# Optimization experiments

Measured on AMD Instinct MI355X. Metric: run time of the kernel, lower is better.

The kernel has to match this reference:

```python
import jax, jax.numpy as jnp
import numpy as np

B, C, L = 4, 192, 4096
DIV = 3
CO = C // DIV  # 64


def setup_inputs() -> dict:
    key = jax.random.key(0)
    ks = jax.random.split(key, 6)
    # kaiming-normal-ish init for 1x1 conv weights, stored as (out, in) matrices
    std = float(np.sqrt(2.0 / C))
    return {
        "x": jax.random.normal(ks[0], (B, C, L, 1), dtype=jnp.float32),
        "Wq": jax.random.normal(ks[1], (CO, C), dtype=jnp.float32) * std,
        "Wk": jax.random.normal(ks[2], (CO, C), dtype=jnp.float32) * std,
        "Wv": jax.random.normal(ks[3], (CO, C), dtype=jnp.float32) * std,
        "Wv1": jax.random.normal(ks[4], (CO, C), dtype=jnp.float32) * std,
        "gamma": jnp.zeros((1,), dtype=jnp.float32) + 0.5,  # nonzero so attn path is exercised
    }


def reference(x, Wq, Wk, Wv, Wv1, gamma):
    b, c, l, _ = x.shape
    xf = x.reshape(b, c, l)                      # (B, C, L)
    f = jnp.einsum("oc,bcl->bol", Wq, xf)        # (B, CO, L)
    g = jnp.einsum("oc,bcl->bol", Wk, xf)
    h = jnp.einsum("oc,bcl->bol", Wv, xf)
    v1 = jnp.einsum("oc,bcl->bol", Wv1, xf)
    # scores[b, l, m] = sum_o f[b,o,l] * g[b,o,m]; softmax over dim=1 (l axis)
    scores = jnp.einsum("bol,bom->blm", f, g)    # (B, L, L)
    beta = jax.nn.softmax(scores, axis=1)
    o = gamma * jnp.einsum("bol,blm->bom", h, beta) + v1  # (B, CO, L)
    return o.reshape(b, c // 3, l, 1)
```

## Files before the change

### kernel.cpp

```cpp
#include <hip/hip_runtime.h>
#include <math.h>

#define B_ 4
#define C_ 192
#define L_ 4096
#define CO_ 64
#define LOG2E 1.44269504088896340736f

using half8 = __attribute__((ext_vector_type(8))) _Float16;
using half4v = __attribute__((ext_vector_type(4))) _Float16;
using half2v = __attribute__((ext_vector_type(2))) _Float16;
using f32x16 = __attribute__((ext_vector_type(16))) float;

#if __has_builtin(__builtin_amdgcn_exp2f)
#define EXP2(x) __builtin_amdgcn_exp2f(x)
#else
#define EXP2(x) exp2f(x)
#endif

__device__ inline half2v pkrtz(float a, float b) {
  return __builtin_bit_cast(half2v, __builtin_amdgcn_cvt_pkrtz(a, b));
}

union U32H2 { int i; half2v h; };
__device__ inline half2v shfl32(half2v v) {
  U32H2 u; u.h = v;
  u.i = __shfl_xor(u.i, 32, 64);
  return u.h;
}


__global__ void wcvt_kernel(const float* __restrict__ Wq,
                            const float* __restrict__ Wk,
                            const float* __restrict__ Wv,
                            const float* __restrict__ Wv1,
                            _Float16* __restrict__ Wf) {
  const float* src = (blockIdx.y == 0) ? Wq
                     : (blockIdx.y == 1) ? Wk
                     : (blockIdx.y == 2) ? Wv : Wv1;
  const float s = (blockIdx.y == 0) ? LOG2E : 1.0f;
  const int idx = (blockIdx.x * 256 + threadIdx.x) * 4;
  if (idx < CO_ * C_) {
    const float4 v = *(const float4*)(src + idx);
    half4v h;
    h[0] = (_Float16)(v.x * s); h[1] = (_Float16)(v.y * s);
    h[2] = (_Float16)(v.z * s); h[3] = (_Float16)(v.w * s);
    *(half4v*)(Wf + (size_t)blockIdx.y * CO_ * C_ + idx) = h;
  }
}

__global__ __launch_bounds__(256) void proj_mfma(
    const float* __restrict__ x, const _Float16* __restrict__ Wf,
    _Float16* __restrict__ fB, _Float16* __restrict__ gB,
    _Float16* __restrict__ hB, float* __restrict__ v1N) {
  __shared__ __align__(16) float xs[C_ * 32];
  const int b = blockIdx.y, l0 = blockIdx.x * 32;
  const int t = threadIdx.x;
  const int lane = t & 63, w = t >> 6;
  const int m = lane & 31, hi = lane >> 5;

  {
    const float* xb = x + (size_t)b * C_ * L_ + l0;
    const int c0 = w * 48;
#pragma unroll
    for (int i = 0; i < 6; ++i) {
      const int cc = c0 + i * 8;
      const float* gp = xb + (size_t)(cc + (lane >> 3)) * L_ + (lane & 7) * 4;
      __builtin_amdgcn_global_load_lds(
          (const __attribute__((address_space(1))) void*)gp,
          (__attribute__((address_space(3))) void*)&xs[cc * 32], 16, 0, 0);
    }
  }
  __syncthreads();

  const _Float16* Wp = Wf + (size_t)w * CO_ * C_;
  if (w < 2) {
    f32x16 acc0 = {}, acc1 = {};
#pragma unroll
    for (int ks = 0; ks < 12; ++ks) {
      const float* xr = &xs[(ks * 16 + hi * 8) * 32 + m];
      half8 aF;
#pragma unroll
      for (int e = 0; e < 8; e += 2) {
        const half2v hp = pkrtz(xr[e * 32], xr[(e + 1) * 32]);
        aF[e] = hp[0]; aF[e + 1] = hp[1];
      }
      const half8 b0 = *(const half8*)(Wp + (size_t)m * C_ + ks * 16 + hi * 8);
      const half8 b1 =
          *(const half8*)(Wp + (size_t)(32 + m) * C_ + ks * 16 + hi * 8);
      acc0 = __builtin_amdgcn_mfma_f32_32x32x16_f16(aF, b0, acc0, 0, 0, 0);
      acc1 = __builtin_amdgcn_mfma_f32_32x32x16_f16(aF, b1, acc1, 0, 0, 0);
    }
    _Float16* dst = (w == 0) ? fB : gB;
#pragma unroll
    for (int r = 0; r < 16; ++r) {
      const int lrow = 4 * hi + 8 * (r >> 2) + (r & 3);
      _Float16* row = dst + ((size_t)b * L_ + l0 + lrow) * CO_;
      row[m] = (_Float16)acc0[r];
      row[32 + m] = (_Float16)acc1[r];
    }
  } else {
    const int lg = l0 + m;
    for (int oh = 0; oh < 2; ++oh) {
      const _Float16* wr = Wp + (size_t)(32 * oh + m) * C_ + hi * 8;
      f32x16 acc = {};
#pragma unroll
      for (int ks = 0; ks < 12; ++ks) {
        const float* xr = &xs[(16 * ks + 8 * hi) * 32 + m];
        half8 bF;
#pragma unroll
        for (int e = 0; e < 8; e += 2) {
          const half2v hp = pkrtz(xr[e * 32], xr[(e + 1) * 32]);
          bF[e] = hp[0]; bF[e + 1] = hp[1];
        }
        const half8 aF = *(const half8*)(wr + ks * 16);
        acc = __builtin_amdgcn_mfma_f32_32x32x16_f16(aF, bF, acc, 0, 0, 0);
      }
      if (w == 2) {
#pragma unroll
        for (int r = 0; r < 16; ++r) {
          const int o = 32 * oh + 4 * hi + 8 * (r >> 2) + (r & 3);
          hB[((size_t)b * CO_ + o) * L_ + lg] = (_Float16)acc[r];
        }
      } else {
#pragma unroll
        for (int r = 0; r < 16; ++r) {
          const int o = 32 * oh + 4 * hi + 8 * (r >> 2) + (r & 3);
          v1N[((size_t)b * CO_ + o) * L_ + lg] = acc[r];
        }
      }
    }
  }
}

__device__ __forceinline__ void softmax_o(const f32x16& S, float& mx, float& Z,
                                          f32x16& oa, f32x16& ob,
                                          const half8* hc, bool h1) {
  float tmax = S[0];
#pragma unroll
  for (int r = 1; r < 16; ++r) tmax = fmaxf(tmax, S[r]);
  tmax = fmaxf(tmax, __shfl_xor(tmax, 32, 64));
  if (__any(tmax > mx)) {
    const float mnew = fmaxf(mx, tmax);
    const float corr = EXP2(mx - mnew);
    mx = mnew;
    Z *= corr;
#pragma unroll
    for (int r = 0; r < 16; ++r) { oa[r] *= corr; ob[r] *= corr; }
  }
  half2v q[8];
  float zl = 0.f;
#pragma unroll
  for (int j = 0; j < 8; ++j) {
    const float p0 = EXP2(S[2 * j] - mx);
    const float p1 = EXP2(S[2 * j + 1] - mx);
    zl += p0 + p1;
    q[j] = pkrtz(p0, p1);
  }
  Z += zl;
  half2v sq[8];
#pragma unroll
  for (int j = 0; j < 8; ++j) sq[j] = shfl32(q[j]);
  const half2v c0 = h1 ? sq[2] : q[0];
  const half2v c1 = h1 ? sq[3] : q[1];
  const half2v c2 = h1 ? q[2] : sq[0];
  const half2v c3 = h1 ? q[3] : sq[1];
  const half2v c4 = h1 ? sq[6] : q[4];
  const half2v c5 = h1 ? sq[7] : q[5];
  const half2v c6 = h1 ? q[6] : sq[4];
  const half2v c7 = h1 ? q[7] : sq[5];
  half8 bP0, bP1;
  bP0[0] = c0[0]; bP0[1] = c0[1]; bP0[2] = c1[0]; bP0[3] = c1[1];
  bP0[4] = c2[0]; bP0[5] = c2[1]; bP0[6] = c3[0]; bP0[7] = c3[1];
  bP1[0] = c4[0]; bP1[1] = c4[1]; bP1[2] = c5[0]; bP1[3] = c5[1];
  bP1[4] = c6[0]; bP1[5] = c6[1]; bP1[6] = c7[0]; bP1[7] = c7[1];
  oa = __builtin_amdgcn_mfma_f32_32x32x16_f16(hc[0], bP0, oa, 0, 0, 0);
  oa = __builtin_amdgcn_mfma_f32_32x32x16_f16(hc[1], bP1, oa, 0, 0, 0);
  ob = __builtin_amdgcn_mfma_f32_32x32x16_f16(hc[2], bP0, ob, 0, 0, 0);
  ob = __builtin_amdgcn_mfma_f32_32x32x16_f16(hc[3], bP1, ob, 0, 0, 0);
}

__global__ __launch_bounds__(512, 2) void attn_mfma(
    const _Float16* __restrict__ fB, const _Float16* __restrict__ gB,
    const _Float16* __restrict__ hB, const float* __restrict__ v1N,
    const float* __restrict__ gamma_p, float* __restrict__ out) {
  __shared__ float obuf4[4][CO_][65];
  __shared__ float redM[8][64];
  __shared__ float redZ[8][64];

  const int id = blockIdx.x;
  const int b = (id >> 1) & 3;
  const int mt = ((id & 1) << 5) | (id >> 3);
  const int m0 = mt * 64;
  const int t = threadIdx.x;
  const int lane = t & 63, s = t >> 6;
  const int m = lane & 31, hi = lane >> 5;
  const bool h1 = (hi != 0);

  const _Float16* fBase = fB + (size_t)b * L_ * CO_;
  const _Float16* hBase = hB + (size_t)b * CO_ * L_;

  const _Float16* g0 = gB + ((size_t)b * L_ + m0 + m) * CO_ + hi * 8;
  const _Float16* g1 = g0 + (size_t)32 * CO_;
  half8 gf0[4], gf1[4];
#pragma unroll
  for (int ks = 0; ks < 4; ++ks) {
    gf0[ks] = *(const half8*)(g0 + ks * 16);
    gf1[ks] = *(const half8*)(g1 + ks * 16);
  }

  f32x16 o0 = {}, o1 = {}, o2 = {}, o3 = {};
  float mx0 = -1e30f, Z0 = 0.f, mx1 = -1e30f, Z1 = 0.f;

  const int lbase = s * 512;
  half8 fc[2][4], hc[2][4];
  {
    const _Float16* fr = fBase + (size_t)(lbase + m) * CO_ + hi * 8;
#pragma unroll
    for (int ks = 0; ks < 4; ++ks) fc[0][ks] = *(const half8*)(fr + ks * 16);
    const _Float16* hr = hBase + (size_t)m * L_ + lbase + hi * 8;
    const _Float16* hr2 = hr + (size_t)32 * L_;
    hc[0][0] = *(const half8*)(hr);
    hc[0][1] = *(const half8*)(hr + 16);
    hc[0][2] = *(const half8*)(hr2);
    hc[0][3] = *(const half8*)(hr2 + 16);
  }

#pragma unroll 2
  for (int stp = 0; stp < 16; ++stp) {
    const int cur = stp & 1, nxt = cur ^ 1;
    const int lb = lbase + stp * 32;
    {
      const int ln = lb + 32;
      const _Float16* fr = fBase + (size_t)(ln + m) * CO_ + hi * 8;
#pragma unroll
      for (int ks = 0; ks < 4; ++ks) fc[nxt][ks] = *(const half8*)(fr + ks * 16);
      const _Float16* hr = hBase + (size_t)m * L_ + ln + hi * 8;
      const _Float16* hr2 = hr + (size_t)32 * L_;
      hc[nxt][0] = *(const half8*)(hr);
      hc[nxt][1] = *(const half8*)(hr + 16);
      hc[nxt][2] = *(const half8*)(hr2);
      hc[nxt][3] = *(const half8*)(hr2 + 16);
    }
    f32x16 S0 = {}, S1 = {};
#pragma unroll
    for (int ks = 0; ks < 4; ++ks) {
      S0 = __builtin_amdgcn_mfma_f32_32x32x16_f16(fc[cur][ks], gf0[ks], S0, 0, 0, 0);
      S1 = __builtin_amdgcn_mfma_f32_32x32x16_f16(fc[cur][ks], gf1[ks], S1, 0, 0, 0);
    }
    softmax_o(S0, mx0, Z0, o0, o1, hc[cur], h1);
    softmax_o(S1, mx1, Z1, o2, o3, hc[cur], h1);
  }

  Z0 += __shfl_xor(Z0, 32, 64);
  Z1 += __shfl_xor(Z1, 32, 64);
  if (hi == 0) {
    redM[s][m] = mx0; redM[s][m + 32] = mx1;
    redZ[s][m] = Z0;  redZ[s][m + 32] = Z1;
  }
  __syncthreads();
  float M0 = redM[0][m], M1 = redM[0][m + 32];
#pragma unroll
  for (int i = 1; i < 8; ++i) {
    M0 = fmaxf(M0, redM[i][m]);
    M1 = fmaxf(M1, redM[i][m + 32]);
  }
  const float sc0 = EXP2(mx0 - M0);
  const float sc1 = EXP2(mx1 - M1);
  if (s < 4) {
#pragma unroll
    for (int r = 0; r < 16; ++r) {
      const int o = 4 * hi + 8 * (r >> 2) + (r & 3);
      obuf4[s][o][m] = sc0 * o0[r];
      obuf4[s][o + 32][m] = sc0 * o1[r];
      obuf4[s][o][m + 32] = sc1 * o2[r];
      obuf4[s][o + 32][m + 32] = sc1 * o3[r];
    }
  }
  __syncthreads();
  if (s >= 4) {
#pragma unroll
    for (int r = 0; r < 16; ++r) {
      const int o = 4 * hi + 8 * (r >> 2) + (r & 3);
      obuf4[s - 4][o][m] += sc0 * o0[r];
      obuf4[s - 4][o + 32][m] += sc0 * o1[r];
      obuf4[s - 4][o][m + 32] += sc1 * o2[r];
      obuf4[s - 4][o + 32][m + 32] += sc1 * o3[r];
    }
  }
  __syncthreads();

  const float gam = gamma_p[0];
  const int me = t & 63;
  const int og = t >> 6;
  float M = redM[0][me];
#pragma unroll
  for (int i = 1; i < 8; ++i) M = fmaxf(M, redM[i][me]);
  float Zt = 0.f;
#pragma unroll
  for (int i = 0; i < 8; ++i) Zt += EXP2(redM[i][me] - M) * redZ[i][me];
  const float inv = 1.0f / Zt;
#pragma unroll
  for (int i = 0; i < 8; ++i) {
    const int o = og * 8 + i;
    const float val = obuf4[0][o][me] + obuf4[1][o][me] +
                      obuf4[2][o][me] + obuf4[3][o][me];
    const size_t g = ((size_t)b * CO_ + o) * L_ + m0 + me;
    out[g] = gam * val * inv + v1N[g];
  }
}

extern "C" void kernel_launch(void* const* d_in, const int* in_sizes, int n_in,
                              void* d_out, int out_size, void* d_ws,
                              size_t ws_size, hipStream_t stream) {
  const float* x = (const float*)d_in[0];
  const float* Wq = (const float*)d_in[1];
  const float* Wk = (const float*)d_in[2];
  const float* Wv = (const float*)d_in[3];
  const float* Wv1 = (const float*)d_in[4];
  const float* gamma = (const float*)d_in[5];
  float* out = (float*)d_out;

  _Float16* Wf = (_Float16*)d_ws;
  _Float16* fB = Wf + (size_t)4 * CO_ * C_;
  _Float16* gB = fB + (size_t)B_ * L_ * CO_;
  _Float16* hB = gB + (size_t)B_ * L_ * CO_;
  float* v1N = (float*)(hB + (size_t)B_ * L_ * CO_);

  wcvt_kernel<<<dim3(12, 4), 256, 0, stream>>>(Wq, Wk, Wv, Wv1, Wf);
  proj_mfma<<<dim3(L_ / 32, B_), 256, 0, stream>>>(x, Wf, fB, gB, hB, v1N);
  attn_mfma<<<256, 512, 0, stream>>>(fB, gB, hB, v1N, gamma, out);
}
```

Before: 118.7 us.

## Pre-pack f, h and weights into MFMA fragment layout; stage P through LDS

Weights are converted into a lane-major MFMA fragment layout so each lane loads a contiguous half8. The projection kernel also writes f and h in that tile-packed layout through LDS staging, so the attention kernel can read them with fully coalesced per-lane loads. In the attention loop, the cross-half shuffle and select shuffle that built the P operand is replaced by writing P to a per-wave LDS scratch and reading it back as B-operand fragments. This trades VALU shuffle work for LDS traffic and adds extra LDS in both kernels, which may affect occupancy.

```diff
diff --git a/kernel.cpp b/kernel.cpp
--- a/kernel.cpp
+++ b/kernel.cpp
@@ -22,39 +22,41 @@
   return __builtin_bit_cast(half2v, __builtin_amdgcn_cvt_pkrtz(a, b));
 }
 
-union U32H2 { int i; half2v h; };
-__device__ inline half2v shfl32(half2v v) {
-  U32H2 u; u.h = v;
-  u.i = __shfl_xor(u.i, 32, 64);
-  return u.h;
-}
-
-
-__global__ void wcvt_kernel(const float* __restrict__ Wq,
-                            const float* __restrict__ Wk,
-                            const float* __restrict__ Wv,
-                            const float* __restrict__ Wv1,
-                            _Float16* __restrict__ Wf) {
-  const float* src = (blockIdx.y == 0) ? Wq
-                     : (blockIdx.y == 1) ? Wk
-                     : (blockIdx.y == 2) ? Wv : Wv1;
-  const float s = (blockIdx.y == 0) ? LOG2E : 1.0f;
-  const int idx = (blockIdx.x * 256 + threadIdx.x) * 4;
-  if (idx < CO_ * C_) {
-    const float4 v = *(const float4*)(src + idx);
-    half4v h;
-    h[0] = (_Float16)(v.x * s); h[1] = (_Float16)(v.y * s);
-    h[2] = (_Float16)(v.z * s); h[3] = (_Float16)(v.w * s);
-    *(half4v*)(Wf + (size_t)blockIdx.y * CO_ * C_ + idx) = h;
-  }
+
+__global__ __launch_bounds__(256) void wpack_kernel(
+    const float* __restrict__ Wq, const float* __restrict__ Wk,
+    const float* __restrict__ Wv, const float* __restrict__ Wv1,
+    _Float16* __restrict__ Wpack) {
+  const int tid = blockIdx.x * 256 + threadIdx.x;
+  const int w = tid / 1536;
+  const int rem = tid % 1536;
+  const int og = rem / 768;
+  const int ks = (rem % 768) / 64;
+  const int lane = rem % 64;
+  const float* src = (w == 0) ? Wq : (w == 1) ? Wk : (w == 2) ? Wv : Wv1;
+  const float s = (w == 0) ? LOG2E : 1.0f;
+  const int row = og * 32 + (lane & 31);
+  const int col = ks * 16 + (lane >> 5) * 8;
+  const float* p = src + row * C_ + col;
+  const float4 a = *(const float4*)(p);
+  const float4 c = *(const float4*)(p + 4);
+  half8 o;
+  half2v t;
+  t = pkrtz(a.x * s, a.y * s); o[0] = t[0]; o[1] = t[1];
+  t = pkrtz(a.z * s, a.w * s); o[2] = t[0]; o[3] = t[1];
+  t = pkrtz(c.x * s, c.y * s); o[4] = t[0]; o[5] = t[1];
+  t = pkrtz(c.z * s, c.w * s); o[6] = t[0]; o[7] = t[1];
+  *(half8*)(Wpack + (size_t)tid * 8) = o;
 }
 
 __global__ __launch_bounds__(256) void proj_mfma(
-    const float* __restrict__ x, const _Float16* __restrict__ Wf,
-    _Float16* __restrict__ fB, _Float16* __restrict__ gB,
-    _Float16* __restrict__ hB, float* __restrict__ v1N) {
+    const float* __restrict__ x, const _Float16* __restrict__ Wpack,
+    _Float16* __restrict__ fPack, _Float16* __restrict__ gB,
+    _Float16* __restrict__ hPack, float* __restrict__ v1N) {
   __shared__ __align__(16) float xs[C_ * 32];
-  const int b = blockIdx.y, l0 = blockIdx.x * 32;
+  __shared__ __align__(16) _Float16 fl[32 * 72];
+  __shared__ __align__(16) _Float16 hl[64 * 40];
+  const int b = blockIdx.y, T = blockIdx.x, l0 = T * 32;
   const int t = threadIdx.x;
   const int lane = t & 63, w = t >> 6;
   const int m = lane & 31, hi = lane >> 5;
@@ -73,7 +75,14 @@
   }
   __syncthreads();
 
-  const _Float16* Wp = Wf + (size_t)w * CO_ * C_;
+  const _Float16* Wp = Wpack + (size_t)w * 1536 * 8;
+  half8 wf[2][12];
+#pragma unroll
+  for (int og = 0; og < 2; ++og)
+#pragma unroll
+    for (int ks = 0; ks < 12; ++ks)
+      wf[og][ks] = *(const half8*)(Wp + ((size_t)(og * 12 + ks) * 64 + lane) * 8);
+
   if (w < 2) {
     f32x16 acc0 = {}, acc1 = {};
 #pragma unroll
@@ -85,24 +94,35 @@
         const half2v hp = pkrtz(xr[e * 32], xr[(e + 1) * 32]);
         aF[e] = hp[0]; aF[e + 1] = hp[1];
       }
-      const half8 b0 = *(const half8*)(Wp + (size_t)m * C_ + ks * 16 + hi * 8);
-      const half8 b1 =
-          *(const half8*)(Wp + (size_t)(32 + m) * C_ + ks * 16 + hi * 8);
-      acc0 = __builtin_amdgcn_mfma_f32_32x32x16_f16(aF, b0, acc0, 0, 0, 0);
-      acc1 = __builtin_amdgcn_mfma_f32_32x32x16_f16(aF, b1, acc1, 0, 0, 0);
-    }
-    _Float16* dst = (w == 0) ? fB : gB;
-#pragma unroll
-    for (int r = 0; r < 16; ++r) {
-      const int lrow = 4 * hi + 8 * (r >> 2) + (r & 3);
-      _Float16* row = dst + ((size_t)b * L_ + l0 + lrow) * CO_;
-      row[m] = (_Float16)acc0[r];
-      row[32 + m] = (_Float16)acc1[r];
+      acc0 = __builtin_amdgcn_mfma_f32_32x32x16_f16(aF, wf[0][ks], acc0, 0, 0, 0);
+      acc1 = __builtin_amdgcn_mfma_f32_32x32x16_f16(aF, wf[1][ks], acc1, 0, 0, 0);
+    }
+    if (w == 0) {
+#pragma unroll
+      for (int r = 0; r < 16; ++r) {
+        const int l = 4 * hi + 8 * (r >> 2) + (r & 3);
+        fl[l * 72 + m] = (_Float16)acc0[r];
+        fl[l * 72 + 32 + m] = (_Float16)acc1[r];
+      }
+      _Float16* dst = fPack + (size_t)b * L_ * CO_ + (size_t)T * 4 * 64 * 8;
+#pragma unroll
+      for (int ks = 0; ks < 4; ++ks) {
+        const half8 v = *(const half8*)&fl[(lane & 31) * 72 + ks * 16 + (lane >> 5) * 8];
+        *(half8*)(dst + ((size_t)ks * 64 + lane) * 8) = v;
+      }
+    } else {
+      _Float16* dst = gB;
+#pragma unroll
+      for (int r = 0; r < 16; ++r) {
+        const int lrow = 4 * hi + 8 * (r >> 2) + (r & 3);
+        _Float16* row = dst + ((size_t)b * L_ + l0 + lrow) * CO_;
+        row[m] = (_Float16)acc0[r];
+        row[32 + m] = (_Float16)acc1[r];
+      }
     }
   } else {
     const int lg = l0 + m;
     for (int oh = 0; oh < 2; ++oh) {
-      const _Float16* wr = Wp + (size_t)(32 * oh + m) * C_ + hi * 8;
       f32x16 acc = {};
 #pragma unroll
       for (int ks = 0; ks < 12; ++ks) {
@@ -113,14 +133,13 @@
           const half2v hp = pkrtz(xr[e * 32], xr[(e + 1) * 32]);
           bF[e] = hp[0]; bF[e + 1] = hp[1];
         }
-        const half8 aF = *(const half8*)(wr + ks * 16);
-        acc = __builtin_amdgcn_mfma_f32_32x32x16_f16(aF, bF, acc, 0, 0, 0);
+        acc = __builtin_amdgcn_mfma_f32_32x32x16_f16(wf[oh][ks], bF, acc, 0, 0, 0);
       }
       if (w == 2) {
 #pragma unroll
         for (int r = 0; r < 16; ++r) {
           const int o = 32 * oh + 4 * hi + 8 * (r >> 2) + (r & 3);
-          hB[((size_t)b * CO_ + o) * L_ + lg] = (_Float16)acc[r];
+          hl[o * 40 + m] = (_Float16)acc[r];
         }
       } else {
 #pragma unroll
@@ -130,12 +149,23 @@
         }
       }
     }
+    if (w == 2) {
+      _Float16* dst = hPack + (size_t)b * L_ * CO_ + (size_t)T * 4 * 64 * 8;
+#pragma unroll
+      for (int j = 0; j < 4; ++j) {
+        const int oh2 = j >> 1, ks2 = j & 1;
+        const half8 v = *(const half8*)&hl[(32 * oh2 + (lane & 31)) * 40 +
+                                           ks2 * 16 + (lane >> 5) * 8];
+        *(half8*)(dst + ((size_t)j * 64 + lane) * 8) = v;
+      }
+    }
   }
 }
 
 __device__ __forceinline__ void softmax_o(const f32x16& S, float& mx, float& Z,
                                           f32x16& oa, f32x16& ob,
-                                          const half8* hc, bool h1) {
+                                          const half8* hc, _Float16* Pw,
+                                          int m, int hi) {
   float tmax = S[0];
 #pragma unroll
   for (int r = 1; r < 16; ++r) tmax = fmaxf(tmax, S[r]);
@@ -148,32 +178,22 @@
 #pragma unroll
     for (int r = 0; r < 16; ++r) { oa[r] *= corr; ob[r] *= corr; }
   }
-  half2v q[8];
   float zl = 0.f;
 #pragma unroll
-  for (int j = 0; j < 8; ++j) {
-    const float p0 = EXP2(S[2 * j] - mx);
-    const float p1 = EXP2(S[2 * j + 1] - mx);
-    zl += p0 + p1;
-    q[j] = pkrtz(p0, p1);
+  for (int u = 0; u < 4; ++u) {
+    const float p0 = EXP2(S[4 * u + 0] - mx);
+    const float p1 = EXP2(S[4 * u + 1] - mx);
+    const float p2 = EXP2(S[4 * u + 2] - mx);
+    const float p3 = EXP2(S[4 * u + 3] - mx);
+    zl += (p0 + p1) + (p2 + p3);
+    const half2v lo = pkrtz(p0, p1);
+    const half2v hi2 = pkrtz(p2, p3);
+    half4v w4; w4[0] = lo[0]; w4[1] = lo[1]; w4[2] = hi2[0]; w4[3] = hi2[1];
+    *(half4v*)(Pw + m * 40 + 4 * hi + 8 * u) = w4;
   }
   Z += zl;
-  half2v sq[8];
-#pragma unroll
-  for (int j = 0; j < 8; ++j) sq[j] = shfl32(q[j]);
-  const half2v c0 = h1 ? sq[2] : q[0];
-  const half2v c1 = h1 ? sq[3] : q[1];
-  const half2v c2 = h1 ? q[2] : sq[0];
-  const half2v c3 = h1 ? q[3] : sq[1];
-  const half2v c4 = h1 ? sq[6] : q[4];
-  const half2v c5 = h1 ? sq[7] : q[5];
-  const half2v c6 = h1 ? q[6] : sq[4];
-  const half2v c7 = h1 ? q[7] : sq[5];
-  half8 bP0, bP1;
-  bP0[0] = c0[0]; bP0[1] = c0[1]; bP0[2] = c1[0]; bP0[3] = c1[1];
-  bP0[4] = c2[0]; bP0[5] = c2[1]; bP0[6] = c3[0]; bP0[7] = c3[1];
-  bP1[0] = c4[0]; bP1[1] = c4[1]; bP1[2] = c5[0]; bP1[3] = c5[1];
-  bP1[4] = c6[0]; bP1[5] = c6[1]; bP1[6] = c7[0]; bP1[7] = c7[1];
+  const half8 bP0 = *(const half8*)(Pw + m * 40 + 8 * hi);
+  const half8 bP1 = *(const half8*)(Pw + m * 40 + 16 + 8 * hi);
   oa = __builtin_amdgcn_mfma_f32_32x32x16_f16(hc[0], bP0, oa, 0, 0, 0);
   oa = __builtin_amdgcn_mfma_f32_32x32x16_f16(hc[1], bP1, oa, 0, 0, 0);
   ob = __builtin_amdgcn_mfma_f32_32x32x16_f16(hc[2], bP0, ob, 0, 0, 0);
@@ -181,9 +201,10 @@
 }
 
 __global__ __launch_bounds__(512, 2) void attn_mfma(
-    const _Float16* __restrict__ fB, const _Float16* __restrict__ gB,
-    const _Float16* __restrict__ hB, const float* __restrict__ v1N,
+    const _Float16* __restrict__ fPack, const _Float16* __restrict__ gB,
+    const _Float16* __restrict__ hPack, const float* __restrict__ v1N,
     const float* __restrict__ gamma_p, float* __restrict__ out) {
+  __shared__ __align__(16) _Float16 Pl[8][32 * 40];
   __shared__ float obuf4[4][CO_][65];
   __shared__ float redM[8][64];
   __shared__ float redZ[8][64];
@@ -195,10 +216,10 @@
   const int t = threadIdx.x;
   const int lane = t & 63, s = t >> 6;
   const int m = lane & 31, hi = lane >> 5;
-  const bool h1 = (hi != 0);
-
-  const _Float16* fBase = fB + (size_t)b * L_ * CO_;
-  const _Float16* hBase = hB + (size_t)b * CO_ * L_;
+
+  const _Float16* fT = fPack + (size_t)b * L_ * CO_;
+  const _Float16* hT = hPack + (size_t)b * L_ * CO_;
+  _Float16* Pw = &Pl[s][0];
 
   const _Float16* g0 = gB + ((size_t)b * L_ + m0 + m) * CO_ + hi * 8;
   const _Float16* g1 = g0 + (size_t)32 * CO_;
@@ -212,35 +233,30 @@
   f32x16 o0 = {}, o1 = {}, o2 = {}, o3 = {};
   float mx0 = -1e30f, Z0 = 0.f, mx1 = -1e30f, Z1 = 0.f;
 
-  const int lbase = s * 512;
+  const int T0 = s * 16;
   half8 fc[2][4], hc[2][4];
   {
-    const _Float16* fr = fBase + (size_t)(lbase + m) * CO_ + hi * 8;
-#pragma unroll
-    for (int ks = 0; ks < 4; ++ks) fc[0][ks] = *(const half8*)(fr + ks * 16);
-    const _Float16* hr = hBase + (size_t)m * L_ + lbase + hi * 8;
-    const _Float16* hr2 = hr + (size_t)32 * L_;
-    hc[0][0] = *(const half8*)(hr);
-    hc[0][1] = *(const half8*)(hr + 16);
-    hc[0][2] = *(const half8*)(hr2);
-    hc[0][3] = *(const half8*)(hr2 + 16);
+    const _Float16* fp = fT + ((size_t)T0 * 4 * 64 + lane) * 8;
+    const _Float16* hp = hT + ((size_t)T0 * 4 * 64 + lane) * 8;
+#pragma unroll
+    for (int ks = 0; ks < 4; ++ks) {
+      fc[0][ks] = *(const half8*)(fp + (size_t)ks * 64 * 8);
+      hc[0][ks] = *(const half8*)(hp + (size_t)ks * 64 * 8);
+    }
   }
 
 #pragma unroll 2
   for (int stp = 0; stp < 16; ++stp) {
     const int cur = stp & 1, nxt = cur ^ 1;
-    const int lb = lbase + stp * 32;
     {
-      const int ln = lb + 32;
-      const _Float16* fr = fBase + (size_t)(ln + m) * CO_ + hi * 8;
-#pragma unroll
-      for (int ks = 0; ks < 4; ++ks) fc[nxt][ks] = *(const half8*)(fr + ks * 16);
-      const _Float16* hr = hBase + (size_t)m * L_ + ln + hi * 8;
-      const _Float16* hr2 = hr + (size_t)32 * L_;
-      hc[nxt][0] = *(const half8*)(hr);
-      hc[nxt][1] = *(const half8*)(hr + 16);
-      hc[nxt][2] = *(const half8*)(hr2);
-      hc[nxt][3] = *(const half8*)(hr2 + 16);
+      const int Tn = T0 + stp + 1;
+      const _Float16* fp = fT + ((size_t)Tn * 4 * 64 + lane) * 8;
+      const _Float16* hp = hT + ((size_t)Tn * 4 * 64 + lane) * 8;
+#pragma unroll
+      for (int ks = 0; ks < 4; ++ks) {
+        fc[nxt][ks] = *(const half8*)(fp + (size_t)ks * 64 * 8);
+        hc[nxt][ks] = *(const half8*)(hp + (size_t)ks * 64 * 8);
+      }
     }
     f32x16 S0 = {}, S1 = {};
 #pragma unroll
@@ -248,8 +264,8 @@
       S0 = __builtin_amdgcn_mfma_f32_32x32x16_f16(fc[cur][ks], gf0[ks], S0, 0, 0, 0);
       S1 = __builtin_amdgcn_mfma_f32_32x32x16_f16(fc[cur][ks], gf1[ks], S1, 0, 0, 0);
     }
-    softmax_o(S0, mx0, Z0, o0, o1, hc[cur], h1);
-    softmax_o(S1, mx1, Z1, o2, o3, hc[cur], h1);
+    softmax_o(S0, mx0, Z0, o0, o1, hc[cur], Pw, m, hi);
+    softmax_o(S1, mx1, Z1, o2, o3, hc[cur], Pw, m, hi);
   }
 
   Z0 += __shfl_xor(Z0, 32, 64);
@@ -321,13 +337,13 @@
   const float* gamma = (const float*)d_in[5];
   float* out = (float*)d_out;
 
-  _Float16* Wf = (_Float16*)d_ws;
-  _Float16* fB = Wf + (size_t)4 * CO_ * C_;
-  _Float16* gB = fB + (size_t)B_ * L_ * CO_;
-  _Float16* hB = gB + (size_t)B_ * L_ * CO_;
-  float* v1N = (float*)(hB + (size_t)B_ * L_ * CO_);
-
-  wcvt_kernel<<<dim3(12, 4), 256, 0, stream>>>(Wq, Wk, Wv, Wv1, Wf);
-  proj_mfma<<<dim3(L_ / 32, B_), 256, 0, stream>>>(x, Wf, fB, gB, hB, v1N);
-  attn_mfma<<<256, 512, 0, stream>>>(fB, gB, hB, v1N, gamma, out);
-}
+  _Float16* Wpack = (_Float16*)d_ws;
+  _Float16* fPack = Wpack + (size_t)4 * 1536 * 8;
+  _Float16* gB = fPack + (size_t)B_ * L_ * CO_;
+  _Float16* hPack = gB + (size_t)B_ * L_ * CO_;
+  float* v1N = (float*)(hPack + (size_t)B_ * L_ * CO_);
+
+  wpack_kernel<<<24, 256, 0, stream>>>(Wq, Wk, Wv, Wv1, Wpack);
+  proj_mfma<<<dim3(L_ / 32, B_), 256, 0, stream>>>(x, Wpack, fPack, gB, hPack, v1N);
+  attn_mfma<<<256, 512, 0, stream>>>(fPack, gB, hPack, v1N, gamma, out);
+}
```

After: 105.6 us. 11.0% less time.
